# Performance work log

Hardware: AMD Instinct MI355X
Metric: run time of the kernel (lower is better)

## Reference

```python
import jax, jax.numpy as jnp
import numpy as np

PH, PW = 7, 7  # pooled_height, pooled_width
B, H, W, C, R = 4, 64, 64, 256, 128


def setup_inputs() -> dict:
    key = jax.random.key(0)
    k1, k2, k3 = jax.random.split(key, 3)
    feature_map = jax.random.normal(k1, (B, H, W, C), dtype=jnp.float32)
    # ROIs: (y_min, x_min, y_max, x_max) relative coords; sized so every
    # region has >= PH rows / PW cols (avoids empty-bin -inf edge case).
    start = jax.random.uniform(k2, (B, R, 2), minval=0.0, maxval=0.4)
    extent = jax.random.uniform(k3, (B, R, 2), minval=0.3, maxval=0.55)
    rois = jnp.concatenate([start, start + extent], axis=-1).astype(jnp.float32)
    return {"feature_map": feature_map, "rois": rois}


def _pool_image(fm, rois_img):
    # fm: (H, W, C); rois_img: (R, 4)
    h, w, _ = fm.shape
    # tf.cast(float->int32) truncates; coords are non-negative so == floor
    h0 = jnp.floor(h * rois_img[:, 0]).astype(jnp.int32)
    w0 = jnp.floor(w * rois_img[:, 1]).astype(jnp.int32)
    h1 = jnp.floor(h * rois_img[:, 2]).astype(jnp.int32)
    w1 = jnp.floor(w * rois_img[:, 3]).astype(jnp.int32)
    rh, rw = h1 - h0, w1 - w0
    hstep = jnp.maximum(rh // PH, 1)  # guard: assumes region >= pooled grid
    wstep = jnp.maximum(rw // PW, 1)

    # Map each absolute row/col to its pooled bin (or PH/PW = "outside").
    rel_h = jnp.arange(h)[None, :] - h0[:, None]            # (R, H)
    bin_h = jnp.clip(rel_h // hstep[:, None], 0, PH - 1)     # last bin extends to region end
    row_id = jnp.where((rel_h >= 0) & (rel_h < rh[:, None]), bin_h, PH)
    rel_w = jnp.arange(w)[None, :] - w0[:, None]            # (R, W)
    bin_w = jnp.clip(rel_w // wstep[:, None], 0, PW - 1)
    col_id = jnp.where((rel_w >= 0) & (rel_w < rw[:, None]), bin_w, PW)

    # Stage 1: segment-max over rows -> (R, PH, W, C)
    seg_rows = jax.vmap(
        lambda ids: jax.ops.segment_max(fm, ids, num_segments=PH + 1)
    )(row_id)[:, :PH]

    # Stage 2: segment-max over cols -> (R, PH, PW, C)
    def col_pool(t, ids):  # t: (PH, W, C)
        tt = jnp.swapaxes(t, 0, 1)  # (W, PH, C)
        s = jax.ops.segment_max(tt, ids, num_segments=PW + 1)[:PW]
        return jnp.swapaxes(s, 0, 1)  # (PH, PW, C)

    return jax.vmap(col_pool)(seg_rows, col_id)


def reference(feature_map, rois):
    # (B, R, PH, PW, C)
    return jax.vmap(_pool_image)(feature_map, rois)
```

## Files before the change

### kernel.cpp

```cpp
#include <hip/hip_runtime.h>
#include <math.h>

#define PH 7
#define PW 7
#define BB 4
#define HH 64
#define WW 64
#define CC 256
#define RR 128
#define CH4 (CC / 4)
#define BINS_PER_IMG (RR * PH * PW)
#define NBINS (BB * BINS_PER_IMG)
#define NBLK (NBINS / 4)
#define BLK_PER_IMG (NBLK / 8)
#define P2H 32
#define P2W 32
#define P2_BYTES ((size_t)BB * P2H * P2W * CC * 4)

typedef float f4 __attribute__((ext_vector_type(4)));

__device__ __forceinline__ f4 max4(f4 a, f4 b) {
    f4 r;
    r.x = fmaxf(a.x, b.x); r.y = fmaxf(a.y, b.y);
    r.z = fmaxf(a.z, b.z); r.w = fmaxf(a.w, b.w);
    return r;
}
__device__ __forceinline__ int rfl(int x) { return __builtin_amdgcn_readfirstlane(x); }

__global__ __launch_bounds__(256) void build_p2_kernel(
    const float* __restrict__ fm, float* __restrict__ p2)
{
    const int lane = threadIdx.x & 63;
    const int wave = rfl((int)threadIdx.x >> 6);
    const int bid  = blockIdx.x;
    const int xcd  = bid & 7;
    const int b    = xcd >> 1;
    const int idx  = (xcd & 1) * 128 + (bid >> 3);
    const int local = idx * 4 + wave;
    const int h2 = local >> 5, w2 = local & 31;

    const f4* src = (const f4*)fm + (((size_t)b * HH + 2 * h2) * WW + 2 * w2) * CH4 + lane;
    f4 v0 = src[0], v1 = src[CH4], v2 = src[WW * CH4], v3 = src[WW * CH4 + CH4];
    ((f4*)p2)[((size_t)b * (P2H * P2W) + local) * CH4 + lane] = max4(max4(v0, v1), max4(v2, v3));
}

__global__ __launch_bounds__(256) void ROIPoolingLayer_62079457296467_kernel(
    const float* __restrict__ fm, const float* __restrict__ rois,
    const float* __restrict__ p2, float* __restrict__ out)
{
    const int lane = threadIdx.x & 63;
    const int wave = rfl((int)threadIdx.x >> 6);

    const int bid   = blockIdx.x;
    const int xcd   = bid & 7;
    const int b     = xcd >> 1;
    const int blkin = (xcd & 1) * BLK_PER_IMG + (bid >> 3);
    const int local = blkin * 4 + wave;
    const int r     = local / (PH * PW);
    const int bin   = local - r * (PH * PW);
    const int ph    = bin / PW;
    const int pw    = bin - ph * PW;

    const f4 roi = ((const f4*)rois)[b * RR + r];
    const int h0 = rfl((int)floorf((float)HH * roi.x));
    const int w0 = rfl((int)floorf((float)WW * roi.y));
    const int h1 = rfl((int)floorf((float)HH * roi.z));
    const int w1 = rfl((int)floorf((float)WW * roi.w));
    const int rh = h1 - h0, rw = w1 - w0;
    const int hstep = max(rh / PH, 1), wstep = max(rw / PW, 1);

    int hs = h0 + ph * hstep;
    int he = (ph == PH - 1) ? (h0 + rh) : (hs + hstep);
    he = min(he, h0 + rh);  he = min(he, HH);
    int ws = w0 + pw * wstep;
    int we = (pw == PW - 1) ? (w0 + rw) : (ws + wstep);
    we = min(we, w0 + rw);  we = min(we, WW);

    const f4* fmb = (const f4*)fm + (size_t)b * (HH * WW) * CH4 + lane;
    const f4* p2b = (const f4*)p2 + (size_t)b * (P2H * P2W) * CH4 + lane;
    f4 acc = (f4){-INFINITY, -INFINITY, -INFINITY, -INFINITY};

    if (he > hs && we > ws) {
        const int wbin = we - ws;
        const int h2s = (hs + 1) >> 1, h2e = he >> 1;
        const int w2s = (ws + 1) >> 1, w2e = we >> 1;
        const int n2h = max(h2e - h2s, 0), n2w = max(w2e - w2s, 0);
        const int il0 = 2 * h2s, il1 = max(2 * h2e, il0);
        const int jl0 = 2 * w2s, jl1 = max(2 * w2e, jl0);

        const int nint = n2h * n2w;
        if (nint > 0) {
            const unsigned m = (65536u + (unsigned)n2w - 1) / (unsigned)n2w;
            for (int p = 0; p < nint; p += 8) {
                f4 v[8];
#pragma unroll
                for (int k = 0; k < 8; ++k) {
                    const int pk = min(p + k, nint - 1);
                    const int q  = (int)(((unsigned)pk * m) >> 16);
                    const int c  = pk - q * n2w;
                    const int off = rfl((h2s + q) * P2W + (w2s + c));
                    v[k] = p2b[(size_t)off * CH4];
                }
#pragma unroll
                for (int k = 0; k < 4; ++k) v[k] = max4(v[k], v[k + 4]);
                acc = max4(acc, max4(max4(v[0], v[1]), max4(v[2], v[3])));
            }
        }

        const int t1 = min(il0, he);
        const int b0 = max(il1, hs);
        const int nt = max(t1 - hs, 0), nb = max(he - b0, 0);
        const int nrow = nt + nb;
        const int rowA = nt ? hs : b0, rowB = b0;
        const int nhe = nrow * wbin;
        if (nhe > 0) {
            const unsigned m = (65536u + (unsigned)wbin - 1) / (unsigned)wbin;
            for (int p = 0; p < nhe; p += 8) {
                f4 v[8];
#pragma unroll
                for (int k = 0; k < 8; ++k) {
                    const int pk = min(p + k, nhe - 1);
                    const int q  = (int)(((unsigned)pk * m) >> 16);
                    const int rr2 = q ? rowB : rowA;
                    const int c  = ws + (pk - q * wbin);
                    const int off = rfl(rr2 * WW + c);
                    v[k] = fmb[(size_t)off * CH4];
                }
#pragma unroll
                for (int k = 0; k < 4; ++k) v[k] = max4(v[k], v[k + 4]);
                acc = max4(acc, max4(max4(v[0], v[1]), max4(v[2], v[3])));
            }
        }

        const int ilen = il1 - il0;
        const int nl = max(min(jl0, we) - ws, 0);
        const int nr = max(we - max(jl1, ws), 0);
        const int ncols = nl + nr;
        const int colA = nl ? ws : (we - 1), colB = we - 1;
        const int nve = ilen * ncols;
        if (nve > 0) {
            for (int p = 0; p < nve; p += 8) {
                f4 v[8];
#pragma unroll
                for (int k = 0; k < 8; ++k) {
                    const int pk = min(p + k, nve - 1);
                    const int hh = il0 + ((ncols == 2) ? (pk >> 1) : pk);
                    const int c  = (ncols == 2 && (pk & 1)) ? colB : colA;
                    const int off = rfl(hh * WW + c);
                    v[k] = fmb[(size_t)off * CH4];
                }
#pragma unroll
                for (int k = 0; k < 4; ++k) v[k] = max4(v[k], v[k + 4]);
                acc = max4(acc, max4(max4(v[0], v[1]), max4(v[2], v[3])));
            }
        }
    }

    const size_t gbin = (size_t)b * BINS_PER_IMG + local;
    __builtin_nontemporal_store(acc, (f4*)out + gbin * CH4 + lane);
}

__global__ __launch_bounds__(256) void roi_direct_kernel(
    const float* __restrict__ fm, const float* __restrict__ rois,
    float* __restrict__ out)
{
    const int lane = threadIdx.x & 63;
    const int wave = rfl((int)threadIdx.x >> 6);
    const int bid   = blockIdx.x;
    const int xcd   = bid & 7;
    const int b     = xcd >> 1;
    const int blkin = (xcd & 1) * BLK_PER_IMG + (bid >> 3);
    const int local = blkin * 4 + wave;
    const int r     = local / (PH * PW);
    const int bin   = local - r * (PH * PW);
    const int ph    = bin / PW;
    const int pw    = bin - ph * PW;
    const f4 roi = ((const f4*)rois)[b * RR + r];
    const int h0 = rfl((int)floorf((float)HH * roi.x));
    const int w0 = rfl((int)floorf((float)WW * roi.y));
    const int h1 = rfl((int)floorf((float)HH * roi.z));
    const int w1 = rfl((int)floorf((float)WW * roi.w));
    const int rh = h1 - h0, rw = w1 - w0;
    const int hstep = max(rh / PH, 1), wstep = max(rw / PW, 1);
    int hs = h0 + ph * hstep;
    int he = (ph == PH - 1) ? (h0 + rh) : (hs + hstep);
    he = min(he, h0 + rh);  he = min(he, HH);
    int ws = w0 + pw * wstep;
    int we = (pw == PW - 1) ? (w0 + rw) : (ws + wstep);
    we = min(we, w0 + rw);  we = min(we, WW);
    const int wbin = we - ws, npix = (he - hs) * wbin;
    const f4* fmb = (const f4*)fm + (((size_t)b * HH + hs) * WW + ws) * CH4 + lane;
    f4 acc = (f4){-INFINITY, -INFINITY, -INFINITY, -INFINITY};
    if (npix > 0) {
        const unsigned m = (65536u + (unsigned)wbin - 1) / (unsigned)wbin;
        for (int p = 0; p < npix; p += 8) {
            f4 v[8];
#pragma unroll
            for (int k = 0; k < 8; ++k) {
                const int pk = min(p + k, npix - 1);
                const int q  = (int)(((unsigned)pk * m) >> 16);
                const int off = rfl(q * WW + (pk - q * wbin));
                v[k] = fmb[(size_t)off * CH4];
            }
#pragma unroll
            for (int k = 0; k < 4; ++k) v[k] = max4(v[k], v[k + 4]);
            acc = max4(acc, max4(max4(v[0], v[1]), max4(v[2], v[3])));
        }
    }
    const size_t gbin = (size_t)b * BINS_PER_IMG + local;
    __builtin_nontemporal_store(acc, (f4*)out + gbin * CH4 + lane);
}

extern "C" void kernel_launch(void* const* d_in, const int* in_sizes, int n_in,
                              void* d_out, int out_size, void* d_ws, size_t ws_size,
                              hipStream_t stream) {
    const float* fm   = (const float*)d_in[0];
    const float* rois = (const float*)d_in[1];
    float* out        = (float*)d_out;
    if (ws_size >= P2_BYTES) {
        float* p2 = (float*)d_ws;
        build_p2_kernel<<<1024, 256, 0, stream>>>(fm, p2);
        ROIPoolingLayer_62079457296467_kernel<<<NBLK, 256, 0, stream>>>(fm, rois, p2, out);
    } else {
        roi_direct_kernel<<<NBLK, 256, 0, stream>>>(fm, rois, out);
    }
}
```

Before: 97.03 us.

## Replace 2x2 strided pyramid with full-resolution sliding 2x2 max map

Precomputes a stride-1 overlapping 2x2 max map of the feature map, so each pooling bin covers itself with ceil(h/2)*ceil(w/2) overlapping window reads instead of pyramid interior cells plus separate edge row and column loops. This removes the branchy edge-handling loops and gives uniform address computation. In exchange, the precompute writes a full-size 16 MB buffer instead of a quarter-size one, and bins narrower than 2 fall back to raw reads.

```diff
diff --git a/kernel.cpp b/kernel.cpp
--- a/kernel.cpp
+++ b/kernel.cpp
@@ -13,9 +13,8 @@
 #define NBINS (BB * BINS_PER_IMG)
 #define NBLK (NBINS / 4)
 #define BLK_PER_IMG (NBLK / 8)
-#define P2H 32
-#define P2W 32
-#define P2_BYTES ((size_t)BB * P2H * P2W * CC * 4)
+#define P2S_BYTES ((size_t)BB * HH * WW * CC * 4)
+#define BUILD_BLK 1008
 
 typedef float f4 __attribute__((ext_vector_type(4)));
 
@@ -27,26 +26,37 @@
 }
 __device__ __forceinline__ int rfl(int x) { return __builtin_amdgcn_readfirstlane(x); }
 
-__global__ __launch_bounds__(256) void build_p2_kernel(
-    const float* __restrict__ fm, float* __restrict__ p2)
+__global__ __launch_bounds__(256) void build_p2s_kernel(
+    const float* __restrict__ fm, float* __restrict__ p2s)
 {
     const int lane = threadIdx.x & 63;
     const int wave = rfl((int)threadIdx.x >> 6);
     const int bid  = blockIdx.x;
     const int xcd  = bid & 7;
     const int b    = xcd >> 1;
-    const int idx  = (xcd & 1) * 128 + (bid >> 3);
+    const int idx  = (xcd & 1) * 126 + (bid >> 3);
     const int local = idx * 4 + wave;
-    const int h2 = local >> 5, w2 = local & 31;
-
-    const f4* src = (const f4*)fm + (((size_t)b * HH + 2 * h2) * WW + 2 * w2) * CH4 + lane;
-    f4 v0 = src[0], v1 = src[CH4], v2 = src[WW * CH4], v3 = src[WW * CH4 + CH4];
-    ((f4*)p2)[((size_t)b * (P2H * P2W) + local) * CH4 + lane] = max4(max4(v0, v1), max4(v2, v3));
+    const int h  = local >> 4;
+    const int c0 = (local & 15) * 4;
+
+    const f4* fb = (const f4*)fm + ((size_t)b * HH + h) * WW * CH4 + lane;
+    f4 rm[5];
+#pragma unroll
+    for (int j = 0; j < 5; ++j) {
+        const int c = min(c0 + j, WW - 1);
+        f4 t = fb[(size_t)c * CH4];
+        f4 u = fb[(size_t)(WW + c) * CH4];
+        rm[j] = max4(t, u);
+    }
+    f4* ob = (f4*)p2s + ((size_t)b * HH + h) * WW * CH4 + lane;
+#pragma unroll
+    for (int j = 0; j < 4; ++j)
+        __builtin_nontemporal_store(max4(rm[j], rm[j + 1]), ob + (size_t)(c0 + j) * CH4);
 }
 
 __global__ __launch_bounds__(256) void ROIPoolingLayer_62079457296467_kernel(
     const float* __restrict__ fm, const float* __restrict__ rois,
-    const float* __restrict__ p2, float* __restrict__ out)
+    const float* __restrict__ p2s, float* __restrict__ out)
 {
     const int lane = threadIdx.x & 63;
     const int wave = rfl((int)threadIdx.x >> 6);
@@ -76,83 +86,46 @@
     int we = (pw == PW - 1) ? (w0 + rw) : (ws + wstep);
     we = min(we, w0 + rw);  we = min(we, WW);
 
-    const f4* fmb = (const f4*)fm + (size_t)b * (HH * WW) * CH4 + lane;
-    const f4* p2b = (const f4*)p2 + (size_t)b * (P2H * P2W) * CH4 + lane;
+    const int hbin = he - hs, wbin = we - ws;
     f4 acc = (f4){-INFINITY, -INFINITY, -INFINITY, -INFINITY};
 
-    if (he > hs && we > ws) {
-        const int wbin = we - ws;
-        const int h2s = (hs + 1) >> 1, h2e = he >> 1;
-        const int w2s = (ws + 1) >> 1, w2e = we >> 1;
-        const int n2h = max(h2e - h2s, 0), n2w = max(w2e - w2s, 0);
-        const int il0 = 2 * h2s, il1 = max(2 * h2e, il0);
-        const int jl0 = 2 * w2s, jl1 = max(2 * w2e, jl0);
-
-        const int nint = n2h * n2w;
-        if (nint > 0) {
-            const unsigned m = (65536u + (unsigned)n2w - 1) / (unsigned)n2w;
-            for (int p = 0; p < nint; p += 8) {
-                f4 v[8];
-#pragma unroll
-                for (int k = 0; k < 8; ++k) {
-                    const int pk = min(p + k, nint - 1);
-                    const int q  = (int)(((unsigned)pk * m) >> 16);
-                    const int c  = pk - q * n2w;
-                    const int off = rfl((h2s + q) * P2W + (w2s + c));
-                    v[k] = p2b[(size_t)off * CH4];
-                }
-#pragma unroll
-                for (int k = 0; k < 4; ++k) v[k] = max4(v[k], v[k + 4]);
-                acc = max4(acc, max4(max4(v[0], v[1]), max4(v[2], v[3])));
+    if (hbin >= 2 && wbin >= 2) {
+        const f4* pb = (const f4*)p2s + (size_t)b * (HH * WW) * CH4 + lane;
+        const int nh = (hbin + 1) >> 1, nw = (wbin + 1) >> 1;
+        const int npos = nh * nw;
+        const unsigned m = (65536u + (unsigned)nw - 1) / (unsigned)nw;
+        for (int p = 0; p < npos; p += 8) {
+            f4 v[8];
+#pragma unroll
+            for (int k = 0; k < 8; ++k) {
+                const int pk  = min(p + k, npos - 1);
+                const int i   = (int)(((unsigned)pk * m) >> 16);
+                const int j   = pk - i * nw;
+                const int row = min(hs + 2 * i, he - 2);
+                const int col = min(ws + 2 * j, we - 2);
+                const int off = rfl(row * WW + col);
+                v[k] = pb[(size_t)off * CH4];
             }
+#pragma unroll
+            for (int k = 0; k < 4; ++k) v[k] = max4(v[k], v[k + 4]);
+            acc = max4(acc, max4(max4(v[0], v[1]), max4(v[2], v[3])));
         }
-
-        const int t1 = min(il0, he);
-        const int b0 = max(il1, hs);
-        const int nt = max(t1 - hs, 0), nb = max(he - b0, 0);
-        const int nrow = nt + nb;
-        const int rowA = nt ? hs : b0, rowB = b0;
-        const int nhe = nrow * wbin;
-        if (nhe > 0) {
-            const unsigned m = (65536u + (unsigned)wbin - 1) / (unsigned)wbin;
-            for (int p = 0; p < nhe; p += 8) {
-                f4 v[8];
-#pragma unroll
-                for (int k = 0; k < 8; ++k) {
-                    const int pk = min(p + k, nhe - 1);
-                    const int q  = (int)(((unsigned)pk * m) >> 16);
-                    const int rr2 = q ? rowB : rowA;
-                    const int c  = ws + (pk - q * wbin);
-                    const int off = rfl(rr2 * WW + c);
-                    v[k] = fmb[(size_t)off * CH4];
-                }
-#pragma unroll
-                for (int k = 0; k < 4; ++k) v[k] = max4(v[k], v[k + 4]);
-                acc = max4(acc, max4(max4(v[0], v[1]), max4(v[2], v[3])));
+    } else if (hbin > 0 && wbin > 0) {
+        const f4* fmb = (const f4*)fm + (((size_t)b * HH + hs) * WW + ws) * CH4 + lane;
+        const int npix = hbin * wbin;
+        const unsigned m = (65536u + (unsigned)wbin - 1) / (unsigned)wbin;
+        for (int p = 0; p < npix; p += 8) {
+            f4 v[8];
+#pragma unroll
+            for (int k = 0; k < 8; ++k) {
+                const int pk = min(p + k, npix - 1);
+                const int q  = (int)(((unsigned)pk * m) >> 16);
+                const int off = rfl(q * WW + (pk - q * wbin));
+                v[k] = fmb[(size_t)off * CH4];
             }
-        }
-
-        const int ilen = il1 - il0;
-        const int nl = max(min(jl0, we) - ws, 0);
-        const int nr = max(we - max(jl1, ws), 0);
-        const int ncols = nl + nr;
-        const int colA = nl ? ws : (we - 1), colB = we - 1;
-        const int nve = ilen * ncols;
-        if (nve > 0) {
-            for (int p = 0; p < nve; p += 8) {
-                f4 v[8];
-#pragma unroll
-                for (int k = 0; k < 8; ++k) {
-                    const int pk = min(p + k, nve - 1);
-                    const int hh = il0 + ((ncols == 2) ? (pk >> 1) : pk);
-                    const int c  = (ncols == 2 && (pk & 1)) ? colB : colA;
-                    const int off = rfl(hh * WW + c);
-                    v[k] = fmb[(size_t)off * CH4];
-                }
-#pragma unroll
-                for (int k = 0; k < 4; ++k) v[k] = max4(v[k], v[k + 4]);
-                acc = max4(acc, max4(max4(v[0], v[1]), max4(v[2], v[3])));
-            }
+#pragma unroll
+            for (int k = 0; k < 4; ++k) v[k] = max4(v[k], v[k + 4]);
+            acc = max4(acc, max4(max4(v[0], v[1]), max4(v[2], v[3])));
         }
     }
 
@@ -217,10 +190,10 @@
     const float* fm   = (const float*)d_in[0];
     const float* rois = (const float*)d_in[1];
     float* out        = (float*)d_out;
-    if (ws_size >= P2_BYTES) {
-        float* p2 = (float*)d_ws;
-        build_p2_kernel<<<1024, 256, 0, stream>>>(fm, p2);
-        ROIPoolingLayer_62079457296467_kernel<<<NBLK, 256, 0, stream>>>(fm, rois, p2, out);
+    if (ws_size >= P2S_BYTES) {
+        float* p2s = (float*)d_ws;
+        build_p2s_kernel<<<BUILD_BLK, 256, 0, stream>>>(fm, p2s);
+        ROIPoolingLayer_62079457296467_kernel<<<NBLK, 256, 0, stream>>>(fm, rois, p2s, out);
     } else {
         roi_direct_kernel<<<NBLK, 256, 0, stream>>>(fm, rois, out);
     }
```

Result: faster. 90.96 us (-6.3%).
